# Performance work log

Hardware: AMD Instinct MI355X
Metric: run time of the kernel (lower is better)

## Reference

```python
import jax, jax.numpy as jnp
import numpy as np


def sparsemax(z, axis=0):
    # Standard sparsemax projection onto the simplex (Martins & Astudillo 2016).
    n = z.shape[axis]
    # shift by max for numerical stability (invariant for sparsemax)
    z = z - jnp.max(z, axis=axis, keepdims=True)
    z_sorted = -jnp.sort(-z, axis=axis)  # descending sort along axis
    z_cumsum = jnp.cumsum(z_sorted, axis=axis)
    k_shape = [1] * z.ndim
    k_shape[axis] = n
    k = jnp.arange(1, n + 1, dtype=z.dtype).reshape(k_shape)
    support = (1.0 + k * z_sorted) > z_cumsum  # in-support mask
    k_sup = jnp.sum(support, axis=axis, keepdims=True)  # support size (int)
    # cumsum value at index k_sup-1 along axis
    cs_k = jnp.take_along_axis(z_cumsum, k_sup - 1, axis=axis)
    tau = (cs_k - 1.0) / k_sup.astype(z.dtype)
    return jnp.maximum(z - tau, 0.0)


def setup_inputs() -> dict:
    key = jax.random.key(0)
    k_x, k_a = jax.random.split(key)
    x = jax.random.normal(k_x, (4096, 8192), dtype=jnp.float32)
    a = jnp.asarray(1.0, dtype=jnp.float32)  # nn.Parameter initialized to 1.0
    return {"x": x, "a": a}


def reference(x, a):
    z = -jnp.exp(a) * x
    return sparsemax(z, axis=0)
```

## Files before the change

kernel.cpp:

```cpp
#include <hip/hip_runtime.h>
#include <math.h>


constexpr int ROWS = 4096;
constexpr int COLS = 8192;
constexpr int CAPC = 64;
constexpr int CPAD = 16;

constexpr int PANA = 16;
constexpr int NPA  = ROWS / PANA;
constexpr int PANC = 8;

__global__ __launch_bounds__(1024)
void k_pmax(const float* __restrict__ x, float* __restrict__ pminx)
{
    const int t = threadIdx.x;
    const int b = blockIdx.x;
    const long row0 = (long)b * PANA;

    float m[2][4];
#pragma unroll
    for (int ch = 0; ch < 2; ++ch)
#pragma unroll
        for (int j = 0; j < 4; ++j) m[ch][j] = 3.0e38f;

    for (int r = 0; r < PANA; ++r) {
        const long rb = (row0 + r) * COLS;
#pragma unroll
        for (int ch = 0; ch < 2; ++ch) {
            const int col = ch * 4096 + t * 4;
            const float4 v = *reinterpret_cast<const float4*>(x + rb + col);
            m[ch][0] = fminf(m[ch][0], v.x);
            m[ch][1] = fminf(m[ch][1], v.y);
            m[ch][2] = fminf(m[ch][2], v.z);
            m[ch][3] = fminf(m[ch][3], v.w);
        }
    }
#pragma unroll
    for (int ch = 0; ch < 2; ++ch) {
        float4 o = make_float4(m[ch][0], m[ch][1], m[ch][2], m[ch][3]);
        *reinterpret_cast<float4*>(pminx + (long)b * COLS + ch * 4096 + t * 4) = o;
    }
}

__global__ __launch_bounds__(256)
void k_reduce(const float* __restrict__ pminx, const float* __restrict__ a,
              float* __restrict__ thrx)
{
    __shared__ float red[8][33];
    const int t  = threadIdx.x;
    const int c  = t & 31;
    const int sl = t >> 5;
    const int col = blockIdx.x * 32 + c;

    float m = 3.0e38f;
    for (int p = sl * 32; p < sl * 32 + 32; ++p)
        m = fminf(m, pminx[(long)p * COLS + col]);
    red[sl][c] = m;
    __syncthreads();
    if (t < 32) {
        float mm = red[0][t];
#pragma unroll
        for (int k = 1; k < 8; ++k) mm = fminf(mm, red[k][t]);
        const float s = -expf(a[0]);
        thrx[blockIdx.x * 32 + t] = (s * mm - 1.000002f) / s;
    }
}

__global__ __launch_bounds__(512, 2)
void k_filter(const float* __restrict__ x, const float* __restrict__ a,
              const float* __restrict__ thrx,
              int* __restrict__ cnt, float2* __restrict__ cand)
{
    __shared__ float tl[COLS];
    const int t = threadIdx.x;
    for (int i = t; i < COLS / 4; i += 512)
        reinterpret_cast<float4*>(tl)[i] =
            reinterpret_cast<const float4*>(thrx)[i];
    __syncthreads();

    const long row0 = (long)blockIdx.x * PANC;
    const float s   = -expf(a[0]);

    for (int r = 0; r < PANC; ++r) {
        const int  row = (int)row0 + r;
        const long rb  = (long)row * COLS;
#pragma unroll
        for (int ch = 0; ch < 4; ++ch) {
            const int col = ch * 2048 + t * 4;
            const float4 v  = *reinterpret_cast<const float4*>(x + rb + col);
            const float4 th = *reinterpret_cast<const float4*>(tl + col);
            if (v.x < th.x) { int i = atomicAdd(&cnt[(col + 0) * CPAD], 1);
                if (i < CAPC) cand[(long)(col + 0) * CAPC + i] =
                    make_float2(s * v.x, __int_as_float(row)); }
            if (v.y < th.y) { int i = atomicAdd(&cnt[(col + 1) * CPAD], 1);
                if (i < CAPC) cand[(long)(col + 1) * CAPC + i] =
                    make_float2(s * v.y, __int_as_float(row)); }
            if (v.z < th.z) { int i = atomicAdd(&cnt[(col + 2) * CPAD], 1);
                if (i < CAPC) cand[(long)(col + 2) * CAPC + i] =
                    make_float2(s * v.z, __int_as_float(row)); }
            if (v.w < th.w) { int i = atomicAdd(&cnt[(col + 3) * CPAD], 1);
                if (i < CAPC) cand[(long)(col + 3) * CAPC + i] =
                    make_float2(s * v.w, __int_as_float(row)); }
        }
    }
}

__global__ __launch_bounds__(256, 4)
void k_solve(const int* __restrict__ cnt, const float2* __restrict__ cand,
             const float* __restrict__ x, const float* __restrict__ a,
             float* __restrict__ out)
{
    const int lane = threadIdx.x & 63;
    const int col  = blockIdx.x * 4 + (threadIdx.x >> 6);
    const int K    = cnt[col * CPAD];

    if (K <= CAPC) {
        float v = -3.3e38f; int row = 0;
        if (lane < K) {
            const float2 p = cand[(long)col * CAPC + lane];
            v = p.x; row = __float_as_int(p.y);
        }
        float t = -3.0e38f, prev = 0.f;
        for (int it = 0; it < CAPC + 4; ++it) {
            const bool act = v > t;
            float ss = act ? v : 0.f;
            float sc = act ? 1.f : 0.f;
#pragma unroll
            for (int m = 1; m < 64; m <<= 1) {
                ss += __shfl_xor(ss, m, 64);
                sc += __shfl_xor(sc, m, 64);
            }
            t = (ss - 1.0f) / sc;
            if (sc == prev) break;
            prev = sc;
        }
        if (v > t) out[(long)row * COLS + col] = v - t;
    } else {
        const float s = -expf(a[0]);
        float t = -3.0e38f, prev = 0.f;
        for (int it = 0; it < 256; ++it) {
            float ss = 0.f, sc = 0.f;
            for (int i = 0; i < ROWS / 64; ++i) {
                const float zz = s * x[(long)(lane + i * 64) * COLS + col];
                if (zz > t) { ss += zz; sc += 1.f; }
            }
#pragma unroll
            for (int m = 1; m < 64; m <<= 1) {
                ss += __shfl_xor(ss, m, 64);
                sc += __shfl_xor(sc, m, 64);
            }
            t = (ss - 1.0f) / sc;
            if (sc == prev) break;
            prev = sc;
        }
        for (int i = 0; i < ROWS / 64; ++i) {
            const long r = lane + i * 64;
            const float zz = s * x[r * COLS + col];
            if (zz > t) out[r * COLS + col] = zz - t;
        }
    }
}

extern "C" void kernel_launch(void* const* d_in, const int* in_sizes, int n_in,
                              void* d_out, int out_size, void* d_ws, size_t ws_size,
                              hipStream_t stream) {
    const float* x = (const float*)d_in[0];
    const float* a = (const float*)d_in[1];
    float* out = (float*)d_out;

    char*   ws    = (char*)d_ws;
    int*    cnt   = (int*)ws;
    float*  thrx  = (float*)(ws + 512 * 1024);
    float*  pminx = (float*)(ws + 1024 * 1024);
    float2* cand  = (float2*)(ws + 9 * 1024 * 1024);

    hipMemsetAsync(cnt, 0, COLS * CPAD * sizeof(int), stream);
    hipMemsetAsync(out, 0, (size_t)ROWS * COLS * sizeof(float), stream);
    hipLaunchKernelGGL(k_pmax,   dim3(NPA),        dim3(1024), 0, stream, x, pminx);
    hipLaunchKernelGGL(k_reduce, dim3(COLS / 32),  dim3(256),  0, stream, pminx, a, thrx);
    hipLaunchKernelGGL(k_filter, dim3(ROWS / PANC),dim3(512),  0, stream, x, a, thrx, cnt, cand);
    hipLaunchKernelGGL(k_solve,  dim3(COLS / 4),   dim3(256),  0, stream, cnt, cand, x, a, out);
}
```

Measured before the change: 264.4 us.

## Fold output and counter zeroing into kernels and simplify column-min reduction

```diff
diff --git a/kernel.cpp b/kernel.cpp
--- a/kernel.cpp
+++ b/kernel.cpp
@@ -11,11 +11,18 @@
 constexpr int NPA  = ROWS / PANA;
 constexpr int PANC = 8;
 
+typedef float vfloat4 __attribute__((ext_vector_type(4)));
+
 __global__ __launch_bounds__(1024)
-void k_pmax(const float* __restrict__ x, float* __restrict__ pminx)
+void k_pmax(const float* __restrict__ x, float* __restrict__ pminx,
+            int* __restrict__ cnt)
 {
     const int t = threadIdx.x;
     const int b = blockIdx.x;
+
+    if (t < 128)
+        reinterpret_cast<int4*>(cnt)[b * 128 + t] = make_int4(0, 0, 0, 0);
+
     const long row0 = (long)b * PANA;
 
     float m[2][4];
@@ -47,30 +54,19 @@
 void k_reduce(const float* __restrict__ pminx, const float* __restrict__ a,
               float* __restrict__ thrx)
 {
-    __shared__ float red[8][33];
-    const int t  = threadIdx.x;
-    const int c  = t & 31;
-    const int sl = t >> 5;
-    const int col = blockIdx.x * 32 + c;
-
+    const int col = blockIdx.x * 256 + threadIdx.x;
     float m = 3.0e38f;
-    for (int p = sl * 32; p < sl * 32 + 32; ++p)
+    for (int p = 0; p < NPA; ++p)
         m = fminf(m, pminx[(long)p * COLS + col]);
-    red[sl][c] = m;
-    __syncthreads();
-    if (t < 32) {
-        float mm = red[0][t];
-#pragma unroll
-        for (int k = 1; k < 8; ++k) mm = fminf(mm, red[k][t]);
-        const float s = -expf(a[0]);
-        thrx[blockIdx.x * 32 + t] = (s * mm - 1.000002f) / s;
-    }
+    const float s = -expf(a[0]);
+    thrx[col] = (s * m - 1.000002f) / s;
 }
 
 __global__ __launch_bounds__(512, 2)
-void k_filter(const float* __restrict__ x, const float* __restrict__ a,
-              const float* __restrict__ thrx,
-              int* __restrict__ cnt, float2* __restrict__ cand)
+void k_filterzero(const float* __restrict__ x, const float* __restrict__ a,
+                  const float* __restrict__ thrx,
+                  int* __restrict__ cnt, float2* __restrict__ cand,
+                  float* __restrict__ out)
 {
     __shared__ float tl[COLS];
     const int t = threadIdx.x;
@@ -81,6 +77,7 @@
 
     const long row0 = (long)blockIdx.x * PANC;
     const float s   = -expf(a[0]);
+    const vfloat4 z4 = {0.f, 0.f, 0.f, 0.f};
 
     for (int r = 0; r < PANC; ++r) {
         const int  row = (int)row0 + r;
@@ -90,6 +87,8 @@
             const int col = ch * 2048 + t * 4;
             const float4 v  = *reinterpret_cast<const float4*>(x + rb + col);
             const float4 th = *reinterpret_cast<const float4*>(tl + col);
+            __builtin_nontemporal_store(z4,
+                reinterpret_cast<vfloat4*>(out + rb + col));
             if (v.x < th.x) { int i = atomicAdd(&cnt[(col + 0) * CPAD], 1);
                 if (i < CAPC) cand[(long)(col + 0) * CAPC + i] =
                     make_float2(s * v.x, __int_as_float(row)); }
@@ -175,10 +174,12 @@
     float*  pminx = (float*)(ws + 1024 * 1024);
     float2* cand  = (float2*)(ws + 9 * 1024 * 1024);
 
-    hipMemsetAsync(cnt, 0, COLS * CPAD * sizeof(int), stream);
-    hipMemsetAsync(out, 0, (size_t)ROWS * COLS * sizeof(float), stream);
-    hipLaunchKernelGGL(k_pmax,   dim3(NPA),        dim3(1024), 0, stream, x, pminx);
-    hipLaunchKernelGGL(k_reduce, dim3(COLS / 32),  dim3(256),  0, stream, pminx, a, thrx);
-    hipLaunchKernelGGL(k_filter, dim3(ROWS / PANC),dim3(512),  0, stream, x, a, thrx, cnt, cand);
-    hipLaunchKernelGGL(k_solve,  dim3(COLS / 4),   dim3(256),  0, stream, cnt, cand, x, a, out);
+    hipLaunchKernelGGL(k_pmax,      dim3(NPA),         dim3(1024), 0, stream,
+                       x, pminx, cnt);
+    hipLaunchKernelGGL(k_reduce,    dim3(COLS / 256),  dim3(256),  0, stream,
+                       pminx, a, thrx);
+    hipLaunchKernelGGL(k_filterzero,dim3(ROWS / PANC), dim3(512),  0, stream,
+                       x, a, thrx, cnt, cand, out);
+    hipLaunchKernelGGL(k_solve,     dim3(COLS / 4),    dim3(256),  0, stream,
+                       cnt, cand, x, a, out);
 }
```

Result: slower. 289.3 us (+9.4%).
